# Optimization experiments

Measured on AMD Instinct MI355X. Metric: run time of the kernel, lower is better.

The kernel has to match this reference:

```python
import jax, jax.numpy as jnp
import numpy as np

N = 100000   # nodes
E = 640000   # edges
D = 128      # feature dim
G = 512      # graphs in the batch


def setup_inputs() -> dict:
    key = jax.random.key(0)
    ks = jax.random.split(key, 6)
    x = jax.random.normal(ks[0], (N, D), dtype=jnp.float32)
    edge_index = jax.random.randint(ks[1], (2, E), 0, N, dtype=jnp.int32)
    batch = jnp.sort(jax.random.randint(ks[2], (N,), 0, G, dtype=jnp.int32))
    scale = 1.0 / np.sqrt(D)
    W0 = jax.random.normal(ks[3], (D, D), dtype=jnp.float32) * scale
    W1 = jax.random.normal(ks[4], (D, D), dtype=jnp.float32) * scale
    W2 = jax.random.normal(ks[5], (D, D), dtype=jnp.float32) * scale
    return {"x": x, "edge_index": edge_index, "batch": batch,
            "W0": W0, "W1": W1, "W2": W2}


def gcn_conv(x, W, row, col, n):
    """GCNConv (bias=False): x' = D^-1/2 (A + I) D^-1/2 (x @ W).
    row/col already include self-loops."""
    xw = x @ W                                              # [N, D]
    deg = jax.ops.segment_sum(jnp.ones_like(col, dtype=x.dtype), col,
                              num_segments=n)               # [N]
    dinv = jnp.where(deg > 0, jax.lax.rsqrt(deg), 0.0)
    norm = dinv[row] * dinv[col]                            # [E+N]
    msgs = norm[:, None] * xw[row]                          # gather + scale
    return jax.ops.segment_sum(msgs, col, num_segments=n)   # scatter-add


def reference(x, edge_index, batch, W0, W1, W2):
    n = x.shape[0]
    loops = jnp.arange(n, dtype=edge_index.dtype)
    row = jnp.concatenate([edge_index[0], loops])
    col = jnp.concatenate([edge_index[1], loops])
    # conv_layers[:-1] (no activation between them in forward)
    x = gcn_conv(x, W0, row, col, n)
    x = gcn_conv(x, W1, row, col, n)
    x = jax.nn.leaky_relu(x, negative_slope=0.01)
    x = gcn_conv(x, W2, row, col, n)
    # global_add_pool over graph ids
    return jax.ops.segment_sum(x, batch, num_segments=G)    # [G, D]
```

## Files before the change

### kernel.cpp

```cpp
#include <hip/hip_runtime.h>
#include <hip/hip_bf16.h>

#define FEAT 128

typedef unsigned int uint32;
typedef unsigned short ushort16;
typedef __attribute__((ext_vector_type(8))) short short8;
typedef __attribute__((ext_vector_type(4))) float v4f;
typedef __attribute__((ext_vector_type(2))) float f32x2;

__device__ __forceinline__ ushort16 f2bf(float f) {
    uint32 u = __float_as_uint(f);
    u += 0x7fffu + ((u >> 16) & 1u);
    return (ushort16)(u >> 16);
}
__device__ __forceinline__ float bflo(uint32 u) { return __uint_as_float(u << 16); }
__device__ __forceinline__ float bfhi(uint32 u) { return __uint_as_float(u & 0xffff0000u); }
__device__ __forceinline__ f32x2 up2(uint32 u) { return (f32x2){bflo(u), bfhi(u)}; }

__device__ __forceinline__ void gemm_body(const float* __restrict__ A,
                                          const ushort16* __restrict__ Wt,
                                          ushort16* __restrict__ Ch, int n,
                                          int pairId, int pairStride,
                                          int tile0, int tile1, int t) {
    const int w = t >> 6;
    const int lane = t & 63;
    const int quad = lane >> 4;
    const int l16 = lane & 15;
    const int colBase = (w & 1) * 64;

    short8 wf[4][4];
#pragma unroll
    for (int ct = 0; ct < 4; ct++) {
        const ushort16* wp = Wt + (size_t)(colBase + ct * 16 + l16) * FEAT + quad * 8;
#pragma unroll
        for (int ks = 0; ks < 4; ks++) wf[ct][ks] = *(const short8*)(wp + ks * 32);
    }

    int tile = tile0 + pairId;
    if (tile >= tile1) return;

    auto loadA = [&](int tl, short8 (&a)[4]) {
        const int rowi = tl * 16 + l16;
        if (rowi < n) {
#pragma unroll
            for (int ks = 0; ks < 4; ks++) {
                const float* ap = A + (size_t)rowi * FEAT + quad * 8 + ks * 32;
                float4 f0 = *(const float4*)ap;
                float4 f1 = *(const float4*)(ap + 4);
                short8 v;
                v[0] = f2bf(f0.x); v[1] = f2bf(f0.y); v[2] = f2bf(f0.z); v[3] = f2bf(f0.w);
                v[4] = f2bf(f1.x); v[5] = f2bf(f1.y); v[6] = f2bf(f1.z); v[7] = f2bf(f1.w);
                a[ks] = v;
            }
        } else {
#pragma unroll
            for (int ks = 0; ks < 4; ks++) a[ks] = (short8)0;
        }
    };

    short8 aCur[4];
    loadA(tile, aCur);

    while (tile < tile1) {
        const int nextTile = tile + pairStride;
        short8 aNxt[4];
        if (nextTile < tile1) loadA(nextTile, aNxt);

        v4f acc[4];
#pragma unroll
        for (int ct = 0; ct < 4; ct++) acc[ct] = (v4f)0.f;
#pragma unroll
        for (int ct = 0; ct < 4; ct++)
#pragma unroll
            for (int ks = 0; ks < 4; ks++)
                acc[ct] = __builtin_amdgcn_mfma_f32_16x16x32_bf16(wf[ct][ks], aCur[ks], acc[ct], 0, 0, 0);

        const int rowi = tile * 16 + l16;
        if (rowi < n) {
#pragma unroll
            for (int ct = 0; ct < 4; ct++) {
                uint2 o;
                o.x = (uint32)f2bf(acc[ct][0]) | ((uint32)f2bf(acc[ct][1]) << 16);
                o.y = (uint32)f2bf(acc[ct][2]) | ((uint32)f2bf(acc[ct][3]) << 16);
                *(uint2*)(Ch + (size_t)rowi * FEAT + colBase + ct * 16 + quad * 4) = o;
            }
        }

        tile = nextTile;
#pragma unroll
        for (int ks = 0; ks < 4; ks++) aCur[ks] = aNxt[ks];
    }
}

__global__ __launch_bounds__(256) void pre_kernel(int* __restrict__ counts, int n,
                                                  const float* __restrict__ W0,
                                                  const float* __restrict__ W1,
                                                  ushort16* __restrict__ W01t,
                                                  float* __restrict__ Pbuf,
                                                  int* __restrict__ flagval) {
    int b = blockIdx.x;
    int t = threadIdx.x;
    if (b < 100) {
        int idx = (b * 256 + t) * 4;
        if (idx + 3 < n) {
            *(int4*)(counts + idx) = make_int4(0, 0, 0, 0);
        } else {
            for (int i = idx; i < n; i++) counts[i] = 0;
        }
    } else if (b < 164) {
        __shared__ float sW0[2][FEAT];
        int wb = b - 100;
        int lk = t >> 7;
        int ncol = t & 127;
        int k = wb * 2 + lk;
        sW0[lk][ncol] = W0[(size_t)k * FEAT + ncol];
        __syncthreads();
        float acc = 0.f;
#pragma unroll 4
        for (int j = 0; j < FEAT; j++)
            acc += sW0[lk][j] * W1[(size_t)j * FEAT + ncol];
        W01t[(size_t)ncol * FEAT + k] = f2bf(acc);
    } else if (b < 196) {
        int zb = b - 164;
        float4 z = make_float4(0.f, 0.f, 0.f, 0.f);
        float* p = Pbuf + (size_t)zb * 2048 + t * 8;
        *(float4*)p = z;
        *(float4*)(p + 4) = z;
    } else {
        if (t < 128) flagval[t] = 0;
    }
}

__global__ __launch_bounds__(256) void histgemmA_kernel(const int* __restrict__ col,
                                                        int* __restrict__ counts, int E,
                                                        const float* __restrict__ A,
                                                        const ushort16* __restrict__ Wt,
                                                        ushort16* __restrict__ Ch, int n) {
    const int b = blockIdx.x;
    const int r9 = b % 9;
    const int g9 = b / 9;
    const int t = threadIdx.x;
    if (r9 >= 4) {
        int hb = g9 * 5 + (r9 - 4);
        int id = hb * 256 + t;
        if (id * 4 + 3 < E) {
            int4 c4 = *(const int4*)(col + id * 4);
            atomicAdd(&counts[c4.x], 1);
            atomicAdd(&counts[c4.y], 1);
            atomicAdd(&counts[c4.z], 1);
            atomicAdd(&counts[c4.w], 1);
        } else {
            for (int e = id * 4; e < E; e++) atomicAdd(&counts[col[e]], 1);
        }
        return;
    }
    int gb = g9 * 4 + r9;
    gemm_body(A, Wt, Ch, n, gb * 2 + ((t >> 6) >> 1), 1024, 0, 3125, t);
}

__global__ __launch_bounds__(256) void scan_chain(const int* __restrict__ counts,
                                                  int* __restrict__ flagval,
                                                  int* __restrict__ off, int* __restrict__ nxt,
                                                  float* __restrict__ dinv, int n) {
    __shared__ int s[256];
    __shared__ int sb[256];
    const int b = blockIdx.x;
    const int base = b * 1024;
    const int t = threadIdx.x;
    int c[4];
    int sum = 0;
#pragma unroll
    for (int i = 0; i < 4; i++) {
        int idx = base + t * 4 + i;
        c[i] = (idx < n) ? counts[idx] : 0;
        sum += c[i];
    }
    int v0 = sum;
    s[t] = sum;
    __syncthreads();
    for (int o = 1; o < 256; o <<= 1) {
        int v = (t >= o) ? s[t - o] : 0;
        __syncthreads();
        s[t] += v;
        __syncthreads();
    }
    if (t == 255) atomicExch(&flagval[b], s[255] + 1);
    int lv = 0;
    if (t < b) {
        for (;;) {
            lv = atomicAdd(&flagval[t], 0);
            if (lv != 0) break;
            __builtin_amdgcn_s_sleep(2);
        }
        lv -= 1;
    }
    sb[t] = lv;
    __syncthreads();
    for (int o = 128; o > 0; o >>= 1) {
        if (t < o) sb[t] += sb[t + o];
        __syncthreads();
    }
    const int sBase = sb[0];
    int excl = s[t] - v0 + sBase;
#pragma unroll
    for (int i = 0; i < 4; i++) {
        int idx = base + t * 4 + i;
        if (idx < n) {
            off[idx] = excl;
            nxt[idx] = excl;
            dinv[idx] = rsqrtf((float)(c[i] + 1));
        }
        excl += c[i];
    }
    if (b == gridDim.x - 1 && t == 255) off[n] = excl;
}

__global__ __launch_bounds__(256) void fillgemmB_kernel(const float* __restrict__ A,
                                                        const ushort16* __restrict__ Wt,
                                                        ushort16* __restrict__ Ch, int n,
                                                        const int* __restrict__ row,
                                                        const int* __restrict__ col,
                                                        int* __restrict__ nxt,
                                                        int* __restrict__ srcArr, int E) {
    const int b = blockIdx.x;
    const int r7 = b % 7;
    const int g7 = b / 7;
    const int t = threadIdx.x;
    if (r7 >= 2) {
        int fb = g7 * 5 + (r7 - 2);
        int e = fb * 256 + t;
        if (e < E) {
            int c = col[e], r = row[e];
            int p = atomicAdd(&nxt[c], 1);
            __builtin_nontemporal_store(r, &srcArr[p]);
        }
        return;
    }
    int gb = g7 * 2 + r7;
    gemm_body(A, Wt, Ch, n, gb * 2 + ((t >> 6) >> 1), 2048, 3125, 6250, t);
}

template <int MODE>
__global__ __launch_bounds__(256) void gather_kernel(const int* __restrict__ off,
                                                     const int* __restrict__ srcArr,
                                                     const float* __restrict__ dinv,
                                                     const uint4* __restrict__ table,
                                                     ushort16* __restrict__ Hh, int n) {
    const int t = threadIdx.x;
    const int node = blockIdx.x * 4 + (t >> 6);
    if (node >= n) return;
    const int lane = t & 63;
    const int grp = lane >> 4;
    const int l16 = lane & 15;
    float dc = dinv[node];

    f32x2 acc[4];
    if (grp == 0) {
        uint4 v = table[(size_t)node * 16 + l16];
        if (MODE == 0) {
            f32x2 w0 = (f32x2){dc, dc};
            acc[0] = w0 * up2(v.x);
            acc[1] = w0 * up2(v.y);
            acc[2] = w0 * up2(v.z);
            acc[3] = w0 * up2(v.w);
        } else {
            acc[0] = up2(v.x);
            acc[1] = up2(v.y);
            acc[2] = up2(v.z);
            acc[3] = up2(v.w);
        }
    } else {
#pragma unroll
        for (int j = 0; j < 4; j++) acc[j] = (f32x2){0.f, 0.f};
    }

    int s = off[node], e = off[node + 1];
    int i = s + grp;
    if (MODE == 0) {
        for (; i + 4 < e; i += 8) {
            int r0 = srcArr[i];
            int r1 = srcArr[i + 4];
            uint4 u0 = table[(size_t)r0 * 16 + l16];
            uint4 u1 = table[(size_t)r1 * 16 + l16];
            float f0 = dinv[r0];
            float f1 = dinv[r1];
            f32x2 n0 = (f32x2){f0, f0};
            f32x2 n1 = (f32x2){f1, f1};
            acc[0] += n0 * up2(u0.x);
            acc[1] += n0 * up2(u0.y);
            acc[2] += n0 * up2(u0.z);
            acc[3] += n0 * up2(u0.w);
            acc[0] += n1 * up2(u1.x);
            acc[1] += n1 * up2(u1.y);
            acc[2] += n1 * up2(u1.z);
            acc[3] += n1 * up2(u1.w);
        }
        if (i < e) {
            int r0 = srcArr[i];
            uint4 u0 = table[(size_t)r0 * 16 + l16];
            float f0 = dinv[r0];
            f32x2 n0 = (f32x2){f0, f0};
            acc[0] += n0 * up2(u0.x);
            acc[1] += n0 * up2(u0.y);
            acc[2] += n0 * up2(u0.z);
            acc[3] += n0 * up2(u0.w);
        }
    } else {
        for (; i + 4 < e; i += 8) {
            int r0 = srcArr[i];
            int r1 = srcArr[i + 4];
            uint4 u0 = table[(size_t)r0 * 16 + l16];
            uint4 u1 = table[(size_t)r1 * 16 + l16];
            acc[0] += up2(u0.x) + up2(u1.x);
            acc[1] += up2(u0.y) + up2(u1.y);
            acc[2] += up2(u0.z) + up2(u1.z);
            acc[3] += up2(u0.w) + up2(u1.w);
        }
        if (i < e) {
            int r0 = srcArr[i];
            uint4 u0 = table[(size_t)r0 * 16 + l16];
            acc[0] += up2(u0.x);
            acc[1] += up2(u0.y);
            acc[2] += up2(u0.z);
            acc[3] += up2(u0.w);
        }
    }

    float b[8] = {acc[0].x, acc[0].y, acc[1].x, acc[1].y,
                  acc[2].x, acc[2].y, acc[3].x, acc[3].y};
#pragma unroll
    for (int j = 0; j < 8; j++) {
        b[j] += __shfl_xor(b[j], 16);
        b[j] += __shfl_xor(b[j], 32);
    }

    if (grp == 0) {
        float sc = dc * dc;
        if (MODE == 1) {
#pragma unroll
            for (int j = 0; j < 8; j++) {
                float h = b[j];
                h = (h >= 0.f) ? h : 0.01f * h;
                b[j] = sc * h;
            }
        } else {
#pragma unroll
            for (int j = 0; j < 8; j++) b[j] *= sc;
        }
        uint4 o;
        o.x = (uint32)f2bf(b[0]) | ((uint32)f2bf(b[1]) << 16);
        o.y = (uint32)f2bf(b[2]) | ((uint32)f2bf(b[3]) << 16);
        o.z = (uint32)f2bf(b[4]) | ((uint32)f2bf(b[5]) << 16);
        o.w = (uint32)f2bf(b[6]) | ((uint32)f2bf(b[7]) << 16);
        *(uint4*)(Hh + (size_t)node * FEAT + l16 * 8) = o;
    }
}

__global__ __launch_bounds__(256) void gatherpool_kernel(const int* __restrict__ off,
                                                         const int* __restrict__ srcArr,
                                                         const float* __restrict__ dinv,
                                                         const uint4* __restrict__ table,
                                                         const int* __restrict__ batch,
                                                         float* __restrict__ P, int n) {
    const int t = threadIdx.x;
    const int wave = blockIdx.x * 4 + (t >> 6);
    const int lane = t & 63;
    const int grp = lane >> 4;
    const int l16 = lane & 15;

    const int node0 = wave * 16;
    if (node0 >= n) return;
    const int node1 = min(node0 + 16, n);

    float pacc[8];
#pragma unroll
    for (int j = 0; j < 8; j++) pacc[j] = 0.f;
    int cur = batch[node0];

    for (int node = node0; node < node1; node++) {
        float dc = dinv[node];
        f32x2 acc[4];
        if (grp == 0) {
            uint4 v = table[(size_t)node * 16 + l16];
            acc[0] = up2(v.x);
            acc[1] = up2(v.y);
            acc[2] = up2(v.z);
            acc[3] = up2(v.w);
        } else {
#pragma unroll
            for (int j = 0; j < 4; j++) acc[j] = (f32x2){0.f, 0.f};
        }

        int s = off[node], e = off[node + 1];
        int i = s + grp;
        for (; i + 4 < e; i += 8) {
            int r0 = srcArr[i];
            int r1 = srcArr[i + 4];
            uint4 u0 = table[(size_t)r0 * 16 + l16];
            uint4 u1 = table[(size_t)r1 * 16 + l16];
            acc[0] += up2(u0.x) + up2(u1.x);
            acc[1] += up2(u0.y) + up2(u1.y);
            acc[2] += up2(u0.z) + up2(u1.z);
            acc[3] += up2(u0.w) + up2(u1.w);
        }
        if (i < e) {
            int r0 = srcArr[i];
            uint4 u0 = table[(size_t)r0 * 16 + l16];
            acc[0] += up2(u0.x);
            acc[1] += up2(u0.y);
            acc[2] += up2(u0.z);
            acc[3] += up2(u0.w);
        }

        float b[8] = {acc[0].x, acc[0].y, acc[1].x, acc[1].y,
                      acc[2].x, acc[2].y, acc[3].x, acc[3].y};
#pragma unroll
        for (int j = 0; j < 8; j++) {
            b[j] += __shfl_xor(b[j], 16);
            b[j] += __shfl_xor(b[j], 32);
        }

        int g = batch[node];
        if (g != cur) {
            atomicAdd(&P[(size_t)cur * FEAT + l16 * 8 + 2 * grp], pacc[2 * grp]);
            atomicAdd(&P[(size_t)cur * FEAT + l16 * 8 + 2 * grp + 1], pacc[2 * grp + 1]);
#pragma unroll
            for (int j = 0; j < 8; j++) pacc[j] = 0.f;
            cur = g;
        }
#pragma unroll
        for (int j = 0; j < 8; j++) pacc[j] += dc * b[j];
    }
    atomicAdd(&P[(size_t)cur * FEAT + l16 * 8 + 2 * grp], pacc[2 * grp]);
    atomicAdd(&P[(size_t)cur * FEAT + l16 * 8 + 2 * grp + 1], pacc[2 * grp + 1]);
}

__global__ __launch_bounds__(128) void pgemm_kernel(const float* __restrict__ P,
                                                    const float* __restrict__ W2,
                                                    float* __restrict__ out) {
    __shared__ float sP[FEAT];
    const int g = blockIdx.x;
    const int t = threadIdx.x;
    sP[t] = P[(size_t)g * FEAT + t];
    __syncthreads();
    float o = 0.f;
#pragma unroll 4
    for (int k = 0; k < FEAT; k++) o += sP[k] * W2[(size_t)k * FEAT + t];
    out[(size_t)g * FEAT + t] = o;
}

extern "C" void kernel_launch(void* const* d_in, const int* in_sizes, int n_in,
                              void* d_out, int out_size, void* d_ws, size_t ws_size,
                              hipStream_t stream) {
    const float* x = (const float*)d_in[0];
    const int* ei = (const int*)d_in[1];
    const int* batch = (const int*)d_in[2];
    const float* W0 = (const float*)d_in[3];
    const float* W1 = (const float*)d_in[4];
    const float* W2 = (const float*)d_in[5];
    float* out = (float*)d_out;

    const int N = in_sizes[0] / FEAT;
    const int E = in_sizes[1] / 2;
    const int G = out_size / FEAT;

    const int* rowI = ei;
    const int* colI = ei + E;

    char* ws = (char*)d_ws;
    auto take = [&](size_t bytes) {
        char* p = ws;
        ws += (bytes + 15) & ~(size_t)15;
        return p;
    };
    int* counts    = (int*)take((size_t)N * 4);
    int* off       = (int*)take((size_t)(N + 1) * 4);
    int* nxt       = (int*)take((size_t)N * 4);
    float* dinv    = (float*)take((size_t)N * 4);
    int* flagval   = (int*)take(128 * 4);
    int* srcArr    = (int*)take((size_t)E * 4);
    ushort16* W01t = (ushort16*)take((size_t)16384 * 2);
    float* Pbuf    = (float*)take((size_t)G * FEAT * 4);
    ushort16* bufA = (ushort16*)take((size_t)N * FEAT * 2);
    ushort16* bufB = (ushort16*)take((size_t)N * FEAT * 2);

    const int nb = (N + 1023) / 1024;

    pre_kernel<<<197, 256, 0, stream>>>(counts, N, W0, W1, W01t, Pbuf, flagval);

    histgemmA_kernel<<<128 * 9, 256, 0, stream>>>(colI, counts, E, x, W01t, bufA, N);

    scan_chain<<<nb, 256, 0, stream>>>(counts, flagval, off, nxt, dinv, N);

    fillgemmB_kernel<<<512 * 7, 256, 0, stream>>>(x, W01t, bufA, N,
                                                  rowI, colI, nxt, srcArr, E);

    const int gatBlocks = (N + 3) / 4;
    gather_kernel<0><<<gatBlocks, 256, 0, stream>>>(off, srcArr, dinv,
                                                    (const uint4*)bufA, bufB, N);
    gather_kernel<1><<<gatBlocks, 256, 0, stream>>>(off, srcArr, dinv,
                                                    (const uint4*)bufB, bufA, N);
    const int nWaves = (N + 15) / 16;
    const int poolBlocks = (nWaves + 3) / 4;
    gatherpool_kernel<<<poolBlocks, 256, 0, stream>>>(off, srcArr, dinv,
                                                      (const uint4*)bufA, batch,
                                                      Pbuf, N);
    pgemm_kernel<<<G, 128, 0, stream>>>(Pbuf, W2, out);
}
```

Measured before the change: 325.7 us.

## Fuse scan into fill/gemm launch and pool with final GEMM via flags

Merges the prefix-scan kernel into the CSR-fill/GEMM-B launch. Fill blocks spin on a global counter until all scan blocks finish, while the GEMM blocks run without waiting. Also merges the final pooled GEMM into the gather-pool kernel: the last G blocks wait on a completion counter before reading P and multiplying by W2. This removes two kernel launches and their inter-kernel gaps, but relies on spin-wait inter-block sync that needs forward progress and the flag slots to be zeroed. It also adds atomic polling traffic.

```diff
diff --git a/kernel.cpp b/kernel.cpp
--- a/kernel.cpp
+++ b/kernel.cpp
@@ -159,75 +159,85 @@
     gemm_body(A, Wt, Ch, n, gb * 2 + ((t >> 6) >> 1), 1024, 0, 3125, t);
 }
 
-__global__ __launch_bounds__(256) void scan_chain(const int* __restrict__ counts,
-                                                  int* __restrict__ flagval,
-                                                  int* __restrict__ off, int* __restrict__ nxt,
-                                                  float* __restrict__ dinv, int n) {
-    __shared__ int s[256];
-    __shared__ int sb[256];
+__global__ __launch_bounds__(256) void fusedBuild_kernel(const int* __restrict__ counts,
+                                                         int* __restrict__ flagval,
+                                                         int* __restrict__ off,
+                                                         int* __restrict__ nxt,
+                                                         float* __restrict__ dinv,
+                                                         const float* __restrict__ A,
+                                                         const ushort16* __restrict__ Wt,
+                                                         ushort16* __restrict__ Ch, int n,
+                                                         const int* __restrict__ row,
+                                                         const int* __restrict__ col,
+                                                         int* __restrict__ srcArr, int E,
+                                                         int nb) {
     const int b = blockIdx.x;
-    const int base = b * 1024;
     const int t = threadIdx.x;
-    int c[4];
-    int sum = 0;
-#pragma unroll
-    for (int i = 0; i < 4; i++) {
-        int idx = base + t * 4 + i;
-        c[i] = (idx < n) ? counts[idx] : 0;
-        sum += c[i];
-    }
-    int v0 = sum;
-    s[t] = sum;
-    __syncthreads();
-    for (int o = 1; o < 256; o <<= 1) {
-        int v = (t >= o) ? s[t - o] : 0;
+
+    if (b < nb) {
+        __shared__ int s[256];
+        __shared__ int sb[256];
+        const int base = b * 1024;
+        int c[4];
+        int sum = 0;
+#pragma unroll
+        for (int i = 0; i < 4; i++) {
+            int idx = base + t * 4 + i;
+            c[i] = (idx < n) ? counts[idx] : 0;
+            sum += c[i];
+        }
+        int v0 = sum;
+        s[t] = sum;
         __syncthreads();
-        s[t] += v;
+        for (int o = 1; o < 256; o <<= 1) {
+            int v = (t >= o) ? s[t - o] : 0;
+            __syncthreads();
+            s[t] += v;
+            __syncthreads();
+        }
+        if (t == 255) atomicExch(&flagval[b], s[255] + 1);
+        int lv = 0;
+        if (t < b) {
+            for (;;) {
+                lv = atomicAdd(&flagval[t], 0);
+                if (lv != 0) break;
+                __builtin_amdgcn_s_sleep(2);
+            }
+            lv -= 1;
+        }
+        sb[t] = lv;
         __syncthreads();
-    }
-    if (t == 255) atomicExch(&flagval[b], s[255] + 1);
-    int lv = 0;
-    if (t < b) {
-        for (;;) {
-            lv = atomicAdd(&flagval[t], 0);
-            if (lv != 0) break;
-            __builtin_amdgcn_s_sleep(2);
-        }
-        lv -= 1;
-    }
-    sb[t] = lv;
-    __syncthreads();
-    for (int o = 128; o > 0; o >>= 1) {
-        if (t < o) sb[t] += sb[t + o];
+        for (int o = 128; o > 0; o >>= 1) {
+            if (t < o) sb[t] += sb[t + o];
+            __syncthreads();
+        }
+        const int sBase = sb[0];
+        int excl = s[t] - v0 + sBase;
+#pragma unroll
+        for (int i = 0; i < 4; i++) {
+            int idx = base + t * 4 + i;
+            if (idx < n) {
+                off[idx] = excl;
+                atomicExch(&nxt[idx], excl);
+                dinv[idx] = rsqrtf((float)(c[i] + 1));
+            }
+            excl += c[i];
+        }
+        if (b == nb - 1 && t == 255) off[n] = excl;
         __syncthreads();
-    }
-    const int sBase = sb[0];
-    int excl = s[t] - v0 + sBase;
-#pragma unroll
-    for (int i = 0; i < 4; i++) {
-        int idx = base + t * 4 + i;
-        if (idx < n) {
-            off[idx] = excl;
-            nxt[idx] = excl;
-            dinv[idx] = rsqrtf((float)(c[i] + 1));
-        }
-        excl += c[i];
-    }
-    if (b == gridDim.x - 1 && t == 255) off[n] = excl;
-}
-
-__global__ __launch_bounds__(256) void fillgemmB_kernel(const float* __restrict__ A,
-                                                        const ushort16* __restrict__ Wt,
-                                                        ushort16* __restrict__ Ch, int n,
-                                                        const int* __restrict__ row,
-                                                        const int* __restrict__ col,
-                                                        int* __restrict__ nxt,
-                                                        int* __restrict__ srcArr, int E) {
-    const int b = blockIdx.x;
-    const int r7 = b % 7;
-    const int g7 = b / 7;
-    const int t = threadIdx.x;
+        if (t == 0) atomicAdd(&flagval[120], 1);
+        return;
+    }
+
+    const int bb = b - nb;
+    const int r7 = bb % 7;
+    const int g7 = bb / 7;
     if (r7 >= 2) {
+        if (t == 0) {
+            while (atomicAdd(&flagval[120], 0) < nb) __builtin_amdgcn_s_sleep(8);
+        }
+        __syncthreads();
+        __threadfence();
         int fb = g7 * 5 + (r7 - 2);
         int e = fb * 256 + t;
         if (e < E) {
@@ -357,12 +367,15 @@
     }
 }
 
-__global__ __launch_bounds__(256) void gatherpool_kernel(const int* __restrict__ off,
-                                                         const int* __restrict__ srcArr,
-                                                         const float* __restrict__ dinv,
-                                                         const uint4* __restrict__ table,
-                                                         const int* __restrict__ batch,
-                                                         float* __restrict__ P, int n) {
+__global__ __launch_bounds__(256) void poolgemm_kernel(const int* __restrict__ off,
+                                                       const int* __restrict__ srcArr,
+                                                       const float* __restrict__ dinv,
+                                                       const uint4* __restrict__ table,
+                                                       const int* __restrict__ batch,
+                                                       float* __restrict__ P, int n,
+                                                       int* __restrict__ flagval,
+                                                       const float* __restrict__ W2,
+                                                       float* __restrict__ out, int G) {
     const int t = threadIdx.x;
     const int wave = blockIdx.x * 4 + (t >> 6);
     const int lane = t & 63;
@@ -370,84 +383,92 @@
     const int l16 = lane & 15;
 
     const int node0 = wave * 16;
-    if (node0 >= n) return;
-    const int node1 = min(node0 + 16, n);
-
-    float pacc[8];
-#pragma unroll
-    for (int j = 0; j < 8; j++) pacc[j] = 0.f;
-    int cur = batch[node0];
-
-    for (int node = node0; node < node1; node++) {
-        float dc = dinv[node];
-        f32x2 acc[4];
-        if (grp == 0) {
-            uint4 v = table[(size_t)node * 16 + l16];
-            acc[0] = up2(v.x);
-            acc[1] = up2(v.y);
-            acc[2] = up2(v.z);
-            acc[3] = up2(v.w);
-        } else {
-#pragma unroll
-            for (int j = 0; j < 4; j++) acc[j] = (f32x2){0.f, 0.f};
-        }
-
-        int s = off[node], e = off[node + 1];
-        int i = s + grp;
-        for (; i + 4 < e; i += 8) {
-            int r0 = srcArr[i];
-            int r1 = srcArr[i + 4];
-            uint4 u0 = table[(size_t)r0 * 16 + l16];
-            uint4 u1 = table[(size_t)r1 * 16 + l16];
-            acc[0] += up2(u0.x) + up2(u1.x);
-            acc[1] += up2(u0.y) + up2(u1.y);
-            acc[2] += up2(u0.z) + up2(u1.z);
-            acc[3] += up2(u0.w) + up2(u1.w);
-        }
-        if (i < e) {
-            int r0 = srcArr[i];
-            uint4 u0 = table[(size_t)r0 * 16 + l16];
-            acc[0] += up2(u0.x);
-            acc[1] += up2(u0.y);
-            acc[2] += up2(u0.z);
-            acc[3] += up2(u0.w);
-        }
-
-        float b[8] = {acc[0].x, acc[0].y, acc[1].x, acc[1].y,
-                      acc[2].x, acc[2].y, acc[3].x, acc[3].y};
-#pragma unroll
-        for (int j = 0; j < 8; j++) {
-            b[j] += __shfl_xor(b[j], 16);
-            b[j] += __shfl_xor(b[j], 32);
-        }
-
-        int g = batch[node];
-        if (g != cur) {
-            atomicAdd(&P[(size_t)cur * FEAT + l16 * 8 + 2 * grp], pacc[2 * grp]);
-            atomicAdd(&P[(size_t)cur * FEAT + l16 * 8 + 2 * grp + 1], pacc[2 * grp + 1]);
-#pragma unroll
-            for (int j = 0; j < 8; j++) pacc[j] = 0.f;
-            cur = g;
-        }
-#pragma unroll
-        for (int j = 0; j < 8; j++) pacc[j] += dc * b[j];
-    }
-    atomicAdd(&P[(size_t)cur * FEAT + l16 * 8 + 2 * grp], pacc[2 * grp]);
-    atomicAdd(&P[(size_t)cur * FEAT + l16 * 8 + 2 * grp + 1], pacc[2 * grp + 1]);
-}
-
-__global__ __launch_bounds__(128) void pgemm_kernel(const float* __restrict__ P,
-                                                    const float* __restrict__ W2,
-                                                    float* __restrict__ out) {
+    if (node0 < n) {
+        const int node1 = min(node0 + 16, n);
+        float pacc[8];
+#pragma unroll
+        for (int j = 0; j < 8; j++) pacc[j] = 0.f;
+        int cur = batch[node0];
+
+        for (int node = node0; node < node1; node++) {
+            float dc = dinv[node];
+            f32x2 acc[4];
+            if (grp == 0) {
+                uint4 v = table[(size_t)node * 16 + l16];
+                acc[0] = up2(v.x);
+                acc[1] = up2(v.y);
+                acc[2] = up2(v.z);
+                acc[3] = up2(v.w);
+            } else {
+#pragma unroll
+                for (int j = 0; j < 4; j++) acc[j] = (f32x2){0.f, 0.f};
+            }
+
+            int s = off[node], e = off[node + 1];
+            int i = s + grp;
+            for (; i + 4 < e; i += 8) {
+                int r0 = srcArr[i];
+                int r1 = srcArr[i + 4];
+                uint4 u0 = table[(size_t)r0 * 16 + l16];
+                uint4 u1 = table[(size_t)r1 * 16 + l16];
+                acc[0] += up2(u0.x) + up2(u1.x);
+                acc[1] += up2(u0.y) + up2(u1.y);
+                acc[2] += up2(u0.z) + up2(u1.z);
+                acc[3] += up2(u0.w) + up2(u1.w);
+            }
+            if (i < e) {
+                int r0 = srcArr[i];
+                uint4 u0 = table[(size_t)r0 * 16 + l16];
+                acc[0] += up2(u0.x);
+                acc[1] += up2(u0.y);
+                acc[2] += up2(u0.z);
+                acc[3] += up2(u0.w);
+            }
+
+            float b[8] = {acc[0].x, acc[0].y, acc[1].x, acc[1].y,
+                          acc[2].x, acc[2].y, acc[3].x, acc[3].y};
+#pragma unroll
+            for (int j = 0; j < 8; j++) {
+                b[j] += __shfl_xor(b[j], 16);
+                b[j] += __shfl_xor(b[j], 32);
+            }
+
+            int g = batch[node];
+            if (g != cur) {
+                atomicAdd(&P[(size_t)cur * FEAT + l16 * 8 + 2 * grp], pacc[2 * grp]);
+                atomicAdd(&P[(size_t)cur * FEAT + l16 * 8 + 2 * grp + 1], pacc[2 * grp + 1]);
+#pragma unroll
+                for (int j = 0; j < 8; j++) pacc[j] = 0.f;
+                cur = g;
+            }
+#pragma unroll
+            for (int j = 0; j < 8; j++) pacc[j] += dc * b[j];
+        }
+        atomicAdd(&P[(size_t)cur * FEAT + l16 * 8 + 2 * grp], pacc[2 * grp]);
+        atomicAdd(&P[(size_t)cur * FEAT + l16 * 8 + 2 * grp + 1], pacc[2 * grp + 1]);
+    }
+
+    __syncthreads();
+    if (t == 0) atomicAdd(&flagval[121], 1);
+
+    const int g = (int)blockIdx.x - ((int)gridDim.x - G);
+    if (g < 0) return;
+    const int total = (int)gridDim.x;
+    if (t == 0) {
+        while (atomicAdd(&flagval[121], 0) < total) __builtin_amdgcn_s_sleep(8);
+    }
+    __syncthreads();
+    __threadfence();
+
     __shared__ float sP[FEAT];
-    const int g = blockIdx.x;
-    const int t = threadIdx.x;
-    sP[t] = P[(size_t)g * FEAT + t];
+    if (t < FEAT) sP[t] = atomicAdd(&P[(size_t)g * FEAT + t], 0.0f);
     __syncthreads();
-    float o = 0.f;
+    if (t < FEAT) {
+        float o = 0.f;
 #pragma unroll 4
-    for (int k = 0; k < FEAT; k++) o += sP[k] * W2[(size_t)k * FEAT + t];
-    out[(size_t)g * FEAT + t] = o;
+        for (int k = 0; k < FEAT; k++) o += sP[k] * W2[(size_t)k * FEAT + t];
+        out[(size_t)g * FEAT + t] = o;
+    }
 }
 
 extern "C" void kernel_launch(void* const* d_in, const int* in_sizes, int n_in,
@@ -491,10 +512,9 @@
 
     histgemmA_kernel<<<128 * 9, 256, 0, stream>>>(colI, counts, E, x, W01t, bufA, N);
 
-    scan_chain<<<nb, 256, 0, stream>>>(counts, flagval, off, nxt, dinv, N);
-
-    fillgemmB_kernel<<<512 * 7, 256, 0, stream>>>(x, W01t, bufA, N,
-                                                  rowI, colI, nxt, srcArr, E);
+    fusedBuild_kernel<<<nb + 512 * 7, 256, 0, stream>>>(counts, flagval, off, nxt,
+                                                        dinv, x, W01t, bufA, N,
+                                                        rowI, colI, srcArr, E, nb);
 
     const int gatBlocks = (N + 3) / 4;
     gather_kernel<0><<<gatBlocks, 256, 0, stream>>>(off, srcArr, dinv,
@@ -503,8 +523,7 @@
                                                     (const uint4*)bufB, bufA, N);
     const int nWaves = (N + 15) / 16;
     const int poolBlocks = (nWaves + 3) / 4;
-    gatherpool_kernel<<<poolBlocks, 256, 0, stream>>>(off, srcArr, dinv,
-                                                      (const uint4*)bufA, batch,
-                                                      Pbuf, N);
-    pgemm_kernel<<<G, 128, 0, stream>>>(Pbuf, W2, out);
-}
+    poolgemm_kernel<<<poolBlocks, 256, 0, stream>>>(off, srcArr, dinv,
+                                                    (const uint4*)bufA, batch,
+                                                    Pbuf, N, flagval, W2, out, G);
+}
```

After: 700.0 us. 2.15x slower.
